# Kernel tuning notes

Hardware: AMD Instinct MI355X
Metric: run time of the kernel (lower is better)

Reference implementation:

```python
import jax, jax.numpy as jnp
import numpy as np

H = 12  # num_attention_heads


def setup_inputs() -> dict:
    key = jax.random.key(0)
    ks = jax.random.split(key, 7)
    B, T, L, D = 4, 64, 128, 768
    input_ids = jax.random.randint(ks[0], (B, T, L), 0, 30000, dtype=jnp.int32)
    speaker_ids = jax.random.randint(ks[1], (B, T), 0, 8, dtype=jnp.int32)
    token_embeddings = jax.random.normal(ks[2], (B, T, L, D), dtype=jnp.float32)
    edu_embeddings = jax.random.normal(ks[3], (B, T, D), dtype=jnp.float32)
    s = 1.0 / np.sqrt(D)
    Wk = jax.random.normal(ks[4], (D, D), dtype=jnp.float32) * s
    Wv = jax.random.normal(ks[5], (D, D), dtype=jnp.float32) * s
    Wq = jax.random.normal(ks[6], (D, D), dtype=jnp.float32) * s
    return {"input_ids": input_ids, "speaker_ids": speaker_ids,
            "token_embeddings": token_embeddings, "edu_embeddings": edu_embeddings,
            "Wk": Wk, "Wv": Wv, "Wq": Wq}


def reference(input_ids, speaker_ids, token_embeddings, edu_embeddings, Wk, Wv, Wq):
    B, T, L = input_ids.shape
    D = token_embeddings.shape[-1]
    d = D // H
    # per-turn keys/values, split into heads: [B,T,H,d]
    k = (edu_embeddings @ Wk.T).reshape(B, T, H, d)
    v = (edu_embeddings @ Wv.T).reshape(B, T, H, d)
    # per-head outer products k (x) v: [B,T,H,d,d]
    kv = jnp.einsum('bthd,bthe->bthde', k, v)
    # speaker-segmented inclusive prefix sum: M[b,t] = sum_{u<=t, spk[u]==spk[t]} kv[b,u]
    same = speaker_ids[:, None, :] == speaker_ids[:, :, None]        # [B,T(t),T(u)]
    causal = jnp.tril(jnp.ones((T, T), dtype=bool))                  # u <= t (inclusive)
    A = (same & causal).astype(kv.dtype)                             # [B,T,T]
    M = jnp.einsum('btu,buhde->bthde', A, kv)                        # [B,T,H,d,d]
    # token queries attend into their turn's speaker memory matrix
    q = (token_embeddings @ Wq.T).reshape(B, T, L, H, d)
    a = jnp.einsum('btlhd,bthde->btlhe', q, M).reshape(B, T, L, D)
    return token_embeddings + a
```

## Files before the change

kernel.cpp:

```cpp
#include <hip/hip_runtime.h>
#include <hip/hip_bf16.h>

#define NB 4
#define NT 64
#define NL 128
#define ND 768
#define NH 12
#define HD 64

typedef __attribute__((ext_vector_type(8))) short short8;
typedef __attribute__((ext_vector_type(4))) float f32x4;

typedef __attribute__((address_space(3))) unsigned int lds_u32;
typedef __attribute__((address_space(1))) const unsigned int glob_u32;

static __device__ __forceinline__ unsigned short f2b(float x) {
    __hip_bfloat16 h = __float2bfloat16(x);
    return *reinterpret_cast<unsigned short*>(&h);
}
static __device__ __forceinline__ float b2f(unsigned short u) {
    unsigned int v = ((unsigned int)u) << 16;
    union { unsigned int i; float f; } c; c.i = v; return c.f;
}
static __device__ __forceinline__ void gl2lds16(const unsigned short* g, unsigned short* l) {
    __builtin_amdgcn_global_load_lds((glob_u32*)g, (lds_u32*)l, 16, 0, 0);
}

#define TE_C   3145728u
#define WQ_C   3219456u
#define EDU_C  3244032u
#define WK_C   3317760u
#define NCHUNK 3391488u

__global__ __launch_bounds__(256) void conv_bf16(
    const float* __restrict__ te, const float* __restrict__ Wq,
    const float* __restrict__ edu, const float* __restrict__ Wk,
    const float* __restrict__ Wv, unsigned short* __restrict__ dst)
{
    for (size_t c = (size_t)blockIdx.x * 256 + threadIdx.x; c < (size_t)NCHUNK;
         c += (size_t)2048 * 256) {
        const float* s;
        if (c < TE_C)       s = te  + c * 8;
        else if (c < WQ_C)  s = Wq  + (c - TE_C)  * 8;
        else if (c < EDU_C) s = edu + (c - WQ_C)  * 8;
        else if (c < WK_C)  s = Wk  + (c - EDU_C) * 8;
        else                s = Wv  + (c - WK_C)  * 8;
        float4 x = *(const float4*)s;
        float4 y = *(const float4*)(s + 4);
        unsigned short v[8];
        v[0] = f2b(x.x); v[1] = f2b(x.y); v[2] = f2b(x.z); v[3] = f2b(x.w);
        v[4] = f2b(y.x); v[5] = f2b(y.y); v[6] = f2b(y.z); v[7] = f2b(y.w);
        *(short8*)(dst + c * 8) = *(short8*)v;
    }
}

__global__ __launch_bounds__(256) void kvm(
    const unsigned short* __restrict__ edu_b,
    const unsigned short* __restrict__ wk_b,
    const unsigned short* __restrict__ wv_b,
    const int* __restrict__ spk,
    unsigned short* __restrict__ Mt)
{
    const int h = blockIdx.x, b = blockIdx.y, eh = blockIdx.z;

    __shared__ float bucket[8][32][65];
    __shared__ float k_s[64][68];
    __shared__ float v_s[64][36];
    __shared__ __align__(16) unsigned short stage[10240];
    __shared__ int spk_s[64];
    unsigned short* edu_s = stage;
    unsigned short* wk_s  = stage + 4096;
    unsigned short* wv_s  = stage + 8192;

    const int tid = threadIdx.x, lane = tid & 63, wvx = tid >> 6;
    const int lr = lane & 15, lg = lane >> 4, r8 = lane >> 3, l8 = lane & 7;

    { float* p = &bucket[0][0][0];
      for (int i = tid; i < 8 * 32 * 65; i += 256) p[i] = 0.f; }
    if (tid < 64) spk_s[tid] = spk[b * NT + tid];

    const unsigned short* edub = edu_b + (size_t)(b * 64) * ND;
    const unsigned short* wkb  = wk_b + (size_t)(h * 64) * ND;
    const unsigned short* wvb  = wv_b + (size_t)(h * 64 + eh * 32) * ND;

    f32x4 acc_k[4], acc_v[2];
    #pragma unroll
    for (int i = 0; i < 4; i++) acc_k[i] = (f32x4){0.f, 0.f, 0.f, 0.f};
    #pragma unroll
    for (int i = 0; i < 2; i++) acc_v[i] = (f32x4){0.f, 0.f, 0.f, 0.f};

    const int sswz = ((l8 ^ r8) * 8);

    for (int k0 = 0; k0 < ND; k0 += 64) {
        __syncthreads();
        #pragma unroll
        for (int j = 0; j < 5; j++) {
            const int cid = wvx * 5 + j;
            const unsigned short* gs; unsigned short* ls;
            if (cid < 8)       { gs = edub + (size_t)(cid * 8 + r8) * ND;        ls = edu_s + cid * 512; }
            else if (cid < 16) { gs = wkb  + (size_t)((cid - 8) * 8 + r8) * ND;  ls = wk_s + (cid - 8) * 512; }
            else               { gs = wvb  + (size_t)((cid - 16) * 8 + r8) * ND; ls = wv_s + (cid - 16) * 512; }
            gl2lds16(gs + k0 + sswz, ls);
        }
        __syncthreads();
        #pragma unroll
        for (int k32 = 0; k32 < 2; k32++) {
            const int cx = (((k32 * 4 + lg) ^ (lr & 7)) * 8);
            short8 eb = *(const short8*)&edu_s[(wvx * 16 + lr) * 64 + cx];
            #pragma unroll
            for (int jb = 0; jb < 4; jb++) {
                short8 ak = *(const short8*)&wk_s[(jb * 16 + lr) * 64 + cx];
                acc_k[jb] = __builtin_amdgcn_mfma_f32_16x16x32_bf16(ak, eb, acc_k[jb], 0, 0, 0);
            }
            #pragma unroll
            for (int jb = 0; jb < 2; jb++) {
                short8 av = *(const short8*)&wv_s[(jb * 16 + lr) * 64 + cx];
                acc_v[jb] = __builtin_amdgcn_mfma_f32_16x16x32_bf16(av, eb, acc_v[jb], 0, 0, 0);
            }
        }
    }

    {
        const int t = wvx * 16 + lr;
        #pragma unroll
        for (int jb = 0; jb < 4; jb++) *(f32x4*)&k_s[t][jb * 16 + lg * 4] = acc_k[jb];
        #pragma unroll
        for (int jb = 0; jb < 2; jb++) *(f32x4*)&v_s[t][jb * 16 + lg * 4] = acc_v[jb];
    }
    __syncthreads();

    const int e = tid & 31, dg = tid >> 5;
    for (int t = 0; t < NT; t++) {
        const int s = spk_s[t];
        const float vv = v_s[t][e];
        unsigned short tmp[8];
        #pragma unroll
        for (int jj = 0; jj < 8; jj++) {
            float m = bucket[s][e][dg * 8 + jj] + k_s[t][dg * 8 + jj] * vv;
            bucket[s][e][dg * 8 + jj] = m;
            tmp[jj] = f2b(m);
        }
        unsigned short* mpp = Mt + (((size_t)(b * NT + t) * NH + h) * HD + eh * 32 + e) * HD + dg * 8;
        *(short8*)mpp = *(short8*)tmp;
    }
}

__global__ __launch_bounds__(256, 3) void fused_qm(
    const unsigned short* __restrict__ te_b,
    const unsigned short* __restrict__ wq_b,
    const unsigned short* __restrict__ Mt,
    float* __restrict__ out)
{
    const int orig = blockIdx.x;
    const int id   = (orig & 7) * 192 + (orig >> 3);
    const int hp   = id % 6;
    const int bt   = id / 6;

    __shared__ __align__(16) unsigned short smem[26624];
    unsigned short* te_s = smem;
    unsigned short* wq_s = smem + 8192;
    unsigned short* q_s  = smem;
    unsigned short* mt_s = smem + 17408;

    const int tid  = threadIdx.x;
    const int lane = tid & 63;
    const int wvx  = tid >> 6;
    const int lr   = lane & 15;
    const int lg   = lane >> 4;
    const int wm   = wvx >> 1;
    const int wn   = wvx & 1;
    const int r8   = lane >> 3;
    const int l8   = lane & 7;
    const int sswz = ((l8 ^ r8) * 8);

    const unsigned short* teb = te_b + (size_t)bt * NL * ND;
    const unsigned short* wqb = wq_b + (size_t)hp * 128 * ND;

    {
        const unsigned short* mp = Mt + ((size_t)bt * NH + hp * 2) * (HD * HD);
        #pragma unroll
        for (int j = 0; j < 4; j++) {
            const int off = wvx * 2048 + j * 512;
            gl2lds16(mp + off + r8 * 64 + sswz, mt_s + off);
        }
    }

    f32x4 acc[4][4];
    #pragma unroll
    for (int i = 0; i < 4; i++)
        #pragma unroll
        for (int j = 0; j < 4; j++) acc[i][j] = (f32x4){0.f, 0.f, 0.f, 0.f};

    for (int k0 = 0; k0 < ND; k0 += 64) {
        __syncthreads();
        #pragma unroll
        for (int j = 0; j < 4; j++) {
            const int rbase = wvx * 32 + j * 8;
            gl2lds16(teb + (size_t)(rbase + r8) * ND + k0 + sswz, te_s + rbase * 64);
            gl2lds16(wqb + (size_t)(rbase + r8) * ND + k0 + sswz, wq_s + rbase * 64);
        }
        __syncthreads();
        #pragma unroll
        for (int k32 = 0; k32 < 2; k32++) {
            short8 af[4], bf[4];
            #pragma unroll
            for (int tm = 0; tm < 4; tm++) {
                const int row = wm * 64 + tm * 16 + lr;
                af[tm] = *(const short8*)&wq_s[row * 64 + (((k32 * 4 + lg) ^ (row & 7)) * 8)];
            }
            #pragma unroll
            for (int tn = 0; tn < 4; tn++) {
                const int row = wn * 64 + tn * 16 + lr;
                bf[tn] = *(const short8*)&te_s[row * 64 + (((k32 * 4 + lg) ^ (row & 7)) * 8)];
            }
            #pragma unroll
            for (int tm = 0; tm < 4; tm++)
                #pragma unroll
                for (int tn = 0; tn < 4; tn++)
                    acc[tm][tn] = __builtin_amdgcn_mfma_f32_16x16x32_bf16(
                        af[tm], bf[tn], acc[tm][tn], 0, 0, 0);
        }
    }

    __syncthreads();

    #pragma unroll
    for (int tm = 0; tm < 4; tm++) {
        const int d0 = wm * 64 + tm * 16 + lg * 4;
        #pragma unroll
        for (int tn = 0; tn < 4; tn++) {
            const int ltok = wn * 64 + tn * 16 + lr;
            f32x4 a = acc[tm][tn];
            uint2 w2;
            w2.x = (unsigned)f2b(a.x) | ((unsigned)f2b(a.y) << 16);
            w2.y = (unsigned)f2b(a.z) | ((unsigned)f2b(a.w) << 16);
            *(uint2*)&q_s[ltok * 136 + d0] = w2;
        }
    }
    __syncthreads();

    const int h2 = wvx & 1;
    const int lh = wvx >> 1;
    f32x4 acc2[4][4];
    #pragma unroll
    for (int i = 0; i < 4; i++)
        #pragma unroll
        for (int j = 0; j < 4; j++) acc2[i][j] = (f32x4){0.f, 0.f, 0.f, 0.f};

    #pragma unroll
    for (int k32 = 0; k32 < 2; k32++) {
        const int ko = k32 * 32 + lg * 8;
        short8 af[4], bf[4];
        #pragma unroll
        for (int tm = 0; tm < 4; tm++)
            af[tm] = *(const short8*)&q_s[(lh * 64 + tm * 16 + lr) * 136 + h2 * 64 + ko];
        #pragma unroll
        for (int tn = 0; tn < 4; tn++) {
            const int row = h2 * 64 + tn * 16 + lr;
            bf[tn] = *(const short8*)&mt_s[row * 64 + (((k32 * 4 + lg) ^ (row & 7)) * 8)];
        }
        #pragma unroll
        for (int tm = 0; tm < 4; tm++)
            #pragma unroll
            for (int tn = 0; tn < 4; tn++)
                acc2[tm][tn] = __builtin_amdgcn_mfma_f32_16x16x32_bf16(
                    af[tm], bf[tn], acc2[tm][tn], 0, 0, 0);
    }

    float* ob = out + (size_t)bt * NL * ND;
    #pragma unroll
    for (int tm = 0; tm < 4; tm++) {
        const int l0 = lh * 64 + tm * 16 + lg * 4;
        #pragma unroll
        for (int tn = 0; tn < 4; tn++) {
            const int cg = hp * 128 + h2 * 64 + tn * 16 + lr;
            f32x4 a = acc2[tm][tn];
            #pragma unroll
            for (int r = 0; r < 4; r++) {
                size_t gi = (size_t)(l0 + r) * ND + cg;
                ob[gi] = b2f(teb[gi]) + a[r];
            }
        }
    }
}

extern "C" void kernel_launch(void* const* d_in, const int* in_sizes, int n_in,
                              void* d_out, int out_size, void* d_ws, size_t ws_size,
                              hipStream_t stream)
{
    const int*   spk = (const int*)d_in[1];
    const float* te  = (const float*)d_in[2];
    const float* edu = (const float*)d_in[3];
    const float* Wk  = (const float*)d_in[4];
    const float* Wv  = (const float*)d_in[5];
    const float* Wq  = (const float*)d_in[6];
    float* out = (float*)d_out;

    unsigned short* bf    = (unsigned short*)d_ws;
    unsigned short* te_bb = bf;
    unsigned short* wq_bb = bf + 25165824u;
    unsigned short* edu_b = bf + 25755648u;
    unsigned short* wk_bb = bf + 25952256u;
    unsigned short* wv_bb = bf + 26542080u;
    unsigned short* Mtbuf = bf + 27131904u;

    conv_bf16<<<2048,            256, 0, stream>>>(te, Wq, edu, Wk, Wv, bf);
    kvm      <<<dim3(NH, NB, 2), 256, 0, stream>>>(edu_b, wk_bb, wv_bb, spk, Mtbuf);
    fused_qm <<<6 * NT * NB,     256, 0, stream>>>(te_bb, wq_bb, Mtbuf, out);
}
```

Measured before the change: 116.2 us.

## Load fp32 token embeddings directly in fused kernel, drop bf16 pre-conversion pass

The separate conversion kernel no longer converts the large token_embeddings tensor to bf16. Instead, fused_qm loads fp32 tiles straight into LDS with a swizzle and packs them to bf16 in registers via a perm-based pack before the MFMA. The residual add now reads fp32 directly. This removes a full read and write pass over the largest tensor, at the cost of more LDS per block (occupancy bound lowered from 3 to 2) and twice the bytes per tile load, though each of the six head-pair blocks per turn now reads fp32 instead of bf16.

```diff
diff --git a/kernel.cpp b/kernel.cpp
--- a/kernel.cpp
+++ b/kernel.cpp
@@ -18,40 +18,37 @@
     __hip_bfloat16 h = __float2bfloat16(x);
     return *reinterpret_cast<unsigned short*>(&h);
 }
-static __device__ __forceinline__ float b2f(unsigned short u) {
-    unsigned int v = ((unsigned int)u) << 16;
-    union { unsigned int i; float f; } c; c.i = v; return c.f;
-}
-static __device__ __forceinline__ void gl2lds16(const unsigned short* g, unsigned short* l) {
+static __device__ __forceinline__ void gl2lds16(const void* g, void* l) {
     __builtin_amdgcn_global_load_lds((glob_u32*)g, (lds_u32*)l, 16, 0, 0);
 }
-
-#define TE_C   3145728u
-#define WQ_C   3219456u
-#define EDU_C  3244032u
-#define WK_C   3317760u
-#define NCHUNK 3391488u
+static __device__ __forceinline__ unsigned pkbf(float lo, float hi) {
+    union { float f; unsigned u; } a, b; a.f = lo; b.f = hi;
+    return __builtin_amdgcn_perm(b.u, a.u, 0x07060302u);
+}
+
+#define WQ_C   73728u
+#define EDU_C  98304u
+#define WK_C   172032u
+#define NCHUNK 245760u
 
 __global__ __launch_bounds__(256) void conv_bf16(
-    const float* __restrict__ te, const float* __restrict__ Wq,
-    const float* __restrict__ edu, const float* __restrict__ Wk,
-    const float* __restrict__ Wv, unsigned short* __restrict__ dst)
+    const float* __restrict__ Wq, const float* __restrict__ edu,
+    const float* __restrict__ Wk, const float* __restrict__ Wv,
+    unsigned short* __restrict__ dst)
 {
-    for (size_t c = (size_t)blockIdx.x * 256 + threadIdx.x; c < (size_t)NCHUNK;
-         c += (size_t)2048 * 256) {
-        const float* s;
-        if (c < TE_C)       s = te  + c * 8;
-        else if (c < WQ_C)  s = Wq  + (c - TE_C)  * 8;
-        else if (c < EDU_C) s = edu + (c - WQ_C)  * 8;
-        else if (c < WK_C)  s = Wk  + (c - EDU_C) * 8;
-        else                s = Wv  + (c - WK_C)  * 8;
-        float4 x = *(const float4*)s;
-        float4 y = *(const float4*)(s + 4);
-        unsigned short v[8];
-        v[0] = f2b(x.x); v[1] = f2b(x.y); v[2] = f2b(x.z); v[3] = f2b(x.w);
-        v[4] = f2b(y.x); v[5] = f2b(y.y); v[6] = f2b(y.z); v[7] = f2b(y.w);
-        *(short8*)(dst + c * 8) = *(short8*)v;
-    }
+    size_t c = (size_t)blockIdx.x * 256 + threadIdx.x;
+    if (c >= NCHUNK) return;
+    const float* s;
+    if (c < WQ_C)       s = Wq  + c * 8;
+    else if (c < EDU_C) s = edu + (c - WQ_C)  * 8;
+    else if (c < WK_C)  s = Wk  + (c - EDU_C) * 8;
+    else                s = Wv  + (c - WK_C)  * 8;
+    float4 x = *(const float4*)s;
+    float4 y = *(const float4*)(s + 4);
+    unsigned short v[8];
+    v[0] = f2b(x.x); v[1] = f2b(x.y); v[2] = f2b(x.z); v[3] = f2b(x.w);
+    v[4] = f2b(y.x); v[5] = f2b(y.y); v[6] = f2b(y.z); v[7] = f2b(y.w);
+    *(short8*)(dst + c * 8) = *(short8*)v;
 }
 
 __global__ __launch_bounds__(256) void kvm(
@@ -145,8 +142,8 @@
     }
 }
 
-__global__ __launch_bounds__(256, 3) void fused_qm(
-    const unsigned short* __restrict__ te_b,
+__global__ __launch_bounds__(256, 2) void fused_qm(
+    const float* __restrict__ te,
     const unsigned short* __restrict__ wq_b,
     const unsigned short* __restrict__ Mt,
     float* __restrict__ out)
@@ -156,11 +153,11 @@
     const int hp   = id % 6;
     const int bt   = id / 6;
 
-    __shared__ __align__(16) unsigned short smem[26624];
-    unsigned short* te_s = smem;
-    unsigned short* wq_s = smem + 8192;
+    __shared__ __align__(16) unsigned short smem[32768];
+    unsigned short* wq_s = smem;
+    float*          te_s = (float*)(smem + 8192);
+    unsigned short* mt_s = smem + 24576;
     unsigned short* q_s  = smem;
-    unsigned short* mt_s = smem + 17408;
 
     const int tid  = threadIdx.x;
     const int lane = tid & 63;
@@ -171,9 +168,8 @@
     const int wn   = wvx & 1;
     const int r8   = lane >> 3;
     const int l8   = lane & 7;
-    const int sswz = ((l8 ^ r8) * 8);
-
-    const unsigned short* teb = te_b + (size_t)bt * NL * ND;
+
+    const float*          teb = te + (size_t)bt * NL * ND;
     const unsigned short* wqb = wq_b + (size_t)hp * 128 * ND;
 
     {
@@ -181,7 +177,7 @@
         #pragma unroll
         for (int j = 0; j < 4; j++) {
             const int off = wvx * 2048 + j * 512;
-            gl2lds16(mp + off + r8 * 64 + sswz, mt_s + off);
+            gl2lds16(mp + off + r8 * 64 + (l8 ^ r8) * 8, mt_s + off);
         }
     }
 
@@ -196,8 +192,15 @@
         #pragma unroll
         for (int j = 0; j < 4; j++) {
             const int rbase = wvx * 32 + j * 8;
-            gl2lds16(teb + (size_t)(rbase + r8) * ND + k0 + sswz, te_s + rbase * 64);
-            gl2lds16(wqb + (size_t)(rbase + r8) * ND + k0 + sswz, wq_s + rbase * 64);
+            gl2lds16(wqb + (size_t)(rbase + r8) * ND + k0 + (l8 ^ r8) * 8,
+                     wq_s + rbase * 64);
+        }
+        #pragma unroll
+        for (int j = 0; j < 8; j++) {
+            const int rbase = wvx * 32 + j * 4;
+            const int row   = rbase + (lane >> 4);
+            const int c     = (lane & 15) ^ (row & 15);
+            gl2lds16(teb + (size_t)row * ND + k0 + c * 4, te_s + rbase * 64);
         }
         __syncthreads();
         #pragma unroll
@@ -206,12 +209,20 @@
             #pragma unroll
             for (int tm = 0; tm < 4; tm++) {
                 const int row = wm * 64 + tm * 16 + lr;
-                af[tm] = *(const short8*)&wq_s[row * 64 + (((k32 * 4 + lg) ^ (row & 7)) * 8)];
+                af[tm] = *(const short8*)&wq_s[row * 64 + (((k32 * 4 + lg) ^ (lr & 7)) * 8)];
             }
             #pragma unroll
             for (int tn = 0; tn < 4; tn++) {
                 const int row = wn * 64 + tn * 16 + lr;
-                bf[tn] = *(const short8*)&te_s[row * 64 + (((k32 * 4 + lg) ^ (row & 7)) * 8)];
+                const int cg  = k32 * 8 + lg * 2;
+                f32x4 x = *(const f32x4*)&te_s[row * 64 + ((cg ^ lr) * 4)];
+                f32x4 y = *(const f32x4*)&te_s[row * 64 + (((cg + 1) ^ lr) * 4)];
+                union { short8 s; unsigned u[4]; } bb;
+                bb.u[0] = pkbf(x.x, x.y);
+                bb.u[1] = pkbf(x.z, x.w);
+                bb.u[2] = pkbf(y.x, y.y);
+                bb.u[3] = pkbf(y.z, y.w);
+                bf[tn] = bb.s;
             }
             #pragma unroll
             for (int tm = 0; tm < 4; tm++)
@@ -232,8 +243,8 @@
             const int ltok = wn * 64 + tn * 16 + lr;
             f32x4 a = acc[tm][tn];
             uint2 w2;
-            w2.x = (unsigned)f2b(a.x) | ((unsigned)f2b(a.y) << 16);
-            w2.y = (unsigned)f2b(a.z) | ((unsigned)f2b(a.w) << 16);
+            w2.x = pkbf(a.x, a.y);
+            w2.y = pkbf(a.z, a.w);
             *(uint2*)&q_s[ltok * 136 + d0] = w2;
         }
     }
@@ -257,7 +268,7 @@
         #pragma unroll
         for (int tn = 0; tn < 4; tn++) {
             const int row = h2 * 64 + tn * 16 + lr;
-            bf[tn] = *(const short8*)&mt_s[row * 64 + (((k32 * 4 + lg) ^ (row & 7)) * 8)];
+            bf[tn] = *(const short8*)&mt_s[row * 64 + (((k32 * 4 + lg) ^ (lr & 7)) * 8)];
         }
         #pragma unroll
         for (int tm = 0; tm < 4; tm++)
@@ -278,7 +289,7 @@
             #pragma unroll
             for (int r = 0; r < 4; r++) {
                 size_t gi = (size_t)(l0 + r) * ND + cg;
-                ob[gi] = b2f(teb[gi]) + a[r];
+                ob[gi] = teb[gi] + a[r];
             }
         }
     }
@@ -297,14 +308,13 @@
     float* out = (float*)d_out;
 
     unsigned short* bf    = (unsigned short*)d_ws;
-    unsigned short* te_bb = bf;
-    unsigned short* wq_bb = bf + 25165824u;
-    unsigned short* edu_b = bf + 25755648u;
-    unsigned short* wk_bb = bf + 25952256u;
-    unsigned short* wv_bb = bf + 26542080u;
-    unsigned short* Mtbuf = bf + 27131904u;
-
-    conv_bf16<<<2048,            256, 0, stream>>>(te, Wq, edu, Wk, Wv, bf);
+    unsigned short* wq_bb = bf;
+    unsigned short* edu_b = bf + 589824u;
+    unsigned short* wk_bb = bf + 786432u;
+    unsigned short* wv_bb = bf + 1376256u;
+    unsigned short* Mtbuf = bf + 1966080u;
+
+    conv_bf16<<<960,             256, 0, stream>>>(Wq, edu, Wk, Wv, bf);
     kvm      <<<dim3(NH, NB, 2), 256, 0, stream>>>(edu_b, wk_bb, wv_bb, spk, Mtbuf);
-    fused_qm <<<6 * NT * NB,     256, 0, stream>>>(te_bb, wq_bb, Mtbuf, out);
-}
+    fused_qm <<<6 * NT * NB,     256, 0, stream>>>(te, wq_bb, Mtbuf, out);
+}
```

Result: faster. 109.9 us (-5.4%).

## Double-buffer te/Wq LDS tiles in fused_qm to overlap loads with MFMA

Applied to the files above, without the earlier changes.

The K loop of the q-projection GEMM now ping-pongs between two LDS buffers. The next 64-wide K slice is issued via global_load_lds while MFMAs run on the current one, and one of the two barriers per iteration is dropped. LDS per block grows to 80KB, and launch bounds drop from 3 to 2 blocks per CU, trading occupancy for overlap. Swizzle index math is also simplified to use lr&7.

```diff
diff --git a/kernel.cpp b/kernel.cpp
--- a/kernel.cpp
+++ b/kernel.cpp
@@ -22,7 +22,7 @@
     unsigned int v = ((unsigned int)u) << 16;
     union { unsigned int i; float f; } c; c.i = v; return c.f;
 }
-static __device__ __forceinline__ void gl2lds16(const unsigned short* g, unsigned short* l) {
+static __device__ __forceinline__ void gl2lds16(const void* g, void* l) {
     __builtin_amdgcn_global_load_lds((glob_u32*)g, (lds_u32*)l, 16, 0, 0);
 }
 
@@ -145,7 +145,7 @@
     }
 }
 
-__global__ __launch_bounds__(256, 3) void fused_qm(
+__global__ __launch_bounds__(256, 2) void fused_qm(
     const unsigned short* __restrict__ te_b,
     const unsigned short* __restrict__ wq_b,
     const unsigned short* __restrict__ Mt,
@@ -156,11 +156,9 @@
     const int hp   = id % 6;
     const int bt   = id / 6;
 
-    __shared__ __align__(16) unsigned short smem[26624];
-    unsigned short* te_s = smem;
-    unsigned short* wq_s = smem + 8192;
+    __shared__ __align__(16) unsigned short smem[40960];
+    unsigned short* mt_s = smem + 32768;
     unsigned short* q_s  = smem;
-    unsigned short* mt_s = smem + 17408;
 
     const int tid  = threadIdx.x;
     const int lane = tid & 63;
@@ -171,7 +169,7 @@
     const int wn   = wvx & 1;
     const int r8   = lane >> 3;
     const int l8   = lane & 7;
-    const int sswz = ((l8 ^ r8) * 8);
+    const int sswz = (l8 ^ r8) * 8;
 
     const unsigned short* teb = te_b + (size_t)bt * NL * ND;
     const unsigned short* wqb = wq_b + (size_t)hp * 128 * ND;
@@ -191,28 +189,29 @@
         #pragma unroll
         for (int j = 0; j < 4; j++) acc[i][j] = (f32x4){0.f, 0.f, 0.f, 0.f};
 
-    for (int k0 = 0; k0 < ND; k0 += 64) {
-        __syncthreads();
+    auto STAGE = [&](int bb, int k0) {
         #pragma unroll
         for (int j = 0; j < 4; j++) {
             const int rbase = wvx * 32 + j * 8;
-            gl2lds16(teb + (size_t)(rbase + r8) * ND + k0 + sswz, te_s + rbase * 64);
-            gl2lds16(wqb + (size_t)(rbase + r8) * ND + k0 + sswz, wq_s + rbase * 64);
-        }
-        __syncthreads();
+            gl2lds16(teb + (size_t)(rbase + r8) * ND + k0 + sswz,
+                     smem + bb + rbase * 64);
+            gl2lds16(wqb + (size_t)(rbase + r8) * ND + k0 + sswz,
+                     smem + bb + 8192 + rbase * 64);
+        }
+    };
+    auto COMPUTE = [&](int bb) {
+        const unsigned short* tes = smem + bb;
+        const unsigned short* wqs = smem + bb + 8192;
         #pragma unroll
         for (int k32 = 0; k32 < 2; k32++) {
+            const int cx = (((k32 * 4 + lg) ^ (lr & 7)) * 8);
             short8 af[4], bf[4];
             #pragma unroll
-            for (int tm = 0; tm < 4; tm++) {
-                const int row = wm * 64 + tm * 16 + lr;
-                af[tm] = *(const short8*)&wq_s[row * 64 + (((k32 * 4 + lg) ^ (row & 7)) * 8)];
-            }
-            #pragma unroll
-            for (int tn = 0; tn < 4; tn++) {
-                const int row = wn * 64 + tn * 16 + lr;
-                bf[tn] = *(const short8*)&te_s[row * 64 + (((k32 * 4 + lg) ^ (row & 7)) * 8)];
-            }
+            for (int tm = 0; tm < 4; tm++)
+                af[tm] = *(const short8*)&wqs[(wm * 64 + tm * 16 + lr) * 64 + cx];
+            #pragma unroll
+            for (int tn = 0; tn < 4; tn++)
+                bf[tn] = *(const short8*)&tes[(wn * 64 + tn * 16 + lr) * 64 + cx];
             #pragma unroll
             for (int tm = 0; tm < 4; tm++)
                 #pragma unroll
@@ -220,9 +219,18 @@
                     acc[tm][tn] = __builtin_amdgcn_mfma_f32_16x16x32_bf16(
                         af[tm], bf[tn], acc[tm][tn], 0, 0, 0);
         }
-    }
-
+    };
+
+    STAGE(0, 0);
     __syncthreads();
+    for (int k0 = 0; k0 < ND; k0 += 128) {
+        STAGE(16384, k0 + 64);
+        COMPUTE(0);
+        __syncthreads();
+        if (k0 + 128 < ND) STAGE(0, k0 + 128);
+        COMPUTE(16384);
+        __syncthreads();
+    }
 
     #pragma unroll
     for (int tm = 0; tm < 4; tm++) {
@@ -250,15 +258,14 @@
     #pragma unroll
     for (int k32 = 0; k32 < 2; k32++) {
         const int ko = k32 * 32 + lg * 8;
+        const int cx = (((k32 * 4 + lg) ^ (lr & 7)) * 8);
         short8 af[4], bf[4];
         #pragma unroll
         for (int tm = 0; tm < 4; tm++)
             af[tm] = *(const short8*)&q_s[(lh * 64 + tm * 16 + lr) * 136 + h2 * 64 + ko];
         #pragma unroll
-        for (int tn = 0; tn < 4; tn++) {
-            const int row = h2 * 64 + tn * 16 + lr;
-            bf[tn] = *(const short8*)&mt_s[row * 64 + (((k32 * 4 + lg) ^ (row & 7)) * 8)];
-        }
+        for (int tn = 0; tn < 4; tn++)
+            bf[tn] = *(const short8*)&mt_s[(h2 * 64 + tn * 16 + lr) * 64 + cx];
         #pragma unroll
         for (int tm = 0; tm < 4; tm++)
             #pragma unroll
```

Result: no change. 115.5 us (-0.6%).
